# Optimization experiments

Hardware: AMD Instinct MI355X
Metric: run time of the kernel (lower is better)

## Reference

```python
import jax, jax.numpy as jnp
import numpy as np

V, E, H, L, B, T = 20000, 128, 192, 3, 256, 512


def _lstm_dir(x, W_ih, W_hh, b, reverse):
    """One direction of one LSTM layer. x: [B,T,I] -> (outputs [B,T,H], final h [B,H]).
    PyTorch gate order: i, f, g, o. b = b_ih + b_hh (summed, same math)."""
    gx = jnp.einsum('bti,gi->tbg', x, W_ih) + b  # [T,B,4H] input contributions, precomputed
    Wh = W_hh.T                                   # [H,4H]

    def step(carry, g):
        h, c = carry
        z = g + h @ Wh                            # [B,4H]
        i, f, gg, o = jnp.split(z, 4, axis=-1)
        c = jax.nn.sigmoid(f) * c + jax.nn.sigmoid(i) * jnp.tanh(gg)
        h = jax.nn.sigmoid(o) * jnp.tanh(c)
        return (h, c), h

    h0 = jnp.zeros((x.shape[0], H), x.dtype)
    (hT, _), hs = jax.lax.scan(step, (h0, h0), gx, reverse=reverse)
    return hs.transpose(1, 0, 2), hT


def setup_inputs() -> dict:
    key = jax.random.key(0)
    ks = jax.random.split(key, 12)
    k = 1.0 / np.sqrt(H)
    u = lambda kk, shape: jax.random.uniform(kk, shape, jnp.float32, -k, k)
    emb = jax.random.normal(ks[0], (V, E), jnp.float32)
    emb = emb.at[0].set(0.0)  # padding_idx=0
    return {
        'x': jax.random.randint(ks[1], (B, T), 0, V),
        'emb': emb,
        'W_ih0': u(ks[2], (2, 4 * H, E)),        # layer 0, [dir, 4H, E]
        'W_hh0': u(ks[3], (2, 4 * H, H)),
        'b0': u(ks[4], (2, 4 * H)) + u(ks[5], (2, 4 * H)),  # b_ih + b_hh
        'W_ih_r': u(ks[6], (L - 1, 2, 4 * H, 2 * H)),       # layers 1..2 take concat(fwd,bwd)
        'W_hh_r': u(ks[7], (L - 1, 2, 4 * H, H)),
        'b_r': u(ks[8], (L - 1, 2, 4 * H)) + u(ks[9], (L - 1, 2, 4 * H)),
        'fc_w': u(ks[10], (1, 2 * H)),
        'fc_b': u(ks[11], (1,)),
    }


def reference(x, emb, W_ih0, W_hh0, b0, W_ih_r, W_hh_r, b_r, fc_w, fc_b):
    h = emb[x]  # [B,T,E]
    hT_f = hT_b = None
    for l in range(L):
        if l == 0:
            Wi, Wh, bb = W_ih0, W_hh0, b0
        else:
            Wi, Wh, bb = W_ih_r[l - 1], W_hh_r[l - 1], b_r[l - 1]
        out_f, hT_f = _lstm_dir(h, Wi[0], Wh[0], bb[0], reverse=False)
        out_b, hT_b = _lstm_dir(h, Wi[1], Wh[1], bb[1], reverse=True)
        h = jnp.concatenate([out_f, out_b], axis=-1)  # [B,T,2H]
        # inter-layer dropout is inactive at inference
    last = jnp.concatenate([hT_f, hT_b], axis=-1)     # [B,2H]  (hidden[-2], hidden[-1])
    return last @ fc_w.T + fc_b                        # [B,1]
```

## Files before the change

### kernel.cpp

```cpp
#include <hip/hip_runtime.h>
#include <hip/hip_bf16.h>


typedef _Float16 f16;
typedef unsigned int u32;
typedef _Float16 f16x8 __attribute__((ext_vector_type(8)));
typedef float f32x4 __attribute__((ext_vector_type(4)));

__device__ __forceinline__ float sigm(float x) {
  float e = __builtin_amdgcn_exp2f(x * -1.44269504088896f);
  return __builtin_amdgcn_rcpf(1.0f + e);
}
__device__ __forceinline__ float tanh_(float x) {
  float e = __builtin_amdgcn_exp2f(x * -2.88539008177793f);
  return __builtin_fmaf(2.0f, __builtin_amdgcn_rcpf(1.0f + e), -1.0f);
}


__global__ void castk(const float* __restrict__ s, f16* __restrict__ d, int n) {
  int i = blockIdx.x * 256 + threadIdx.x;
  int st = gridDim.x * 256;
  for (; i < n; i += st) d[i] = (f16)s[i];
}

__global__ void castwhh(const float* __restrict__ src, f16* __restrict__ dst) {
  int o = blockIdx.x * 256 + threadIdx.x;
  int e = o & 7, rest = o >> 3;
  int l = rest & 63; rest >>= 6;
  int kk = rest % 6; rest /= 6;
  int g = rest & 3; rest >>= 2;
  int w = rest % 12; int dir = rest / 12;
  int lo16 = l & 15, lhi = l >> 4;
  dst[o] = (f16)src[(size_t)(dir * 768 + g * 192 + w * 16 + lo16) * 192 + kk * 32 + lhi * 8 + e];
}

__global__ void embedk(const int* __restrict__ x, const float* __restrict__ emb,
                       f16* __restrict__ A0) {
  int row = blockIdx.x * 8 + (threadIdx.x >> 5);
  int t = row >> 8, b = row & 255;
  int xi = x[b * 512 + t];
  int c = (threadIdx.x & 31) * 4;
  float4 v = *(const float4*)(emb + (size_t)xi * 128 + c);
  union { f16 h[4]; uint2 u; } p;
  p.h[0] = (f16)v.x; p.h[1] = (f16)v.y; p.h[2] = (f16)v.z; p.h[3] = (f16)v.w;
  *(uint2*)(A0 + (size_t)row * 128 + c) = p.u;
}

template <int KD>
__global__ __launch_bounds__(768)
void fusedk(const f16* __restrict__ in, const f16* __restrict__ Bt,
            const float* __restrict__ bias,
            const u32* __restrict__ gxR, u32* __restrict__ gxW,
            const f16* __restrict__ whh16,
            f16* __restrict__ outh, float* __restrict__ hT,
            f16* __restrict__ carh, float* __restrict__ carc,
            int c, int cg, int NC, int TC, int doLstm, int wOut, int wHT) {
  union SMem {
    struct { uint4 A[1024]; uint4 B[1536]; } g;
    f16 hb[2][16 * 200];
  };
  __shared__ __align__(16) SMem sm;
  const int wg = blockIdx.x;
  const int tid = threadIdx.x;
  const int l = tid & 63, w = tid >> 6;
  const int lo16 = l & 15, lhi = l >> 4;

  if (doLstm && wg < 32) {
    const int dir = wg & 1, bblk = wg >> 1;
    const int u0 = w * 16;
    const int bb = bblk * 16 + lhi * 4;
    const int dc = dir * 192;

    f16x8 wf[4][6];
#pragma unroll
    for (int g = 0; g < 4; ++g)
#pragma unroll
      for (int kk = 0; kk < 6; ++kk)
        wf[g][kk] = *(const f16x8*)(whh16 + ((((size_t)dir * 12 + w) * 4 + g) * 6 + kk) * 512 + l * 8);

    float cq[4];
    if (c == 0) {
      f16* hz = (f16*)sm.hb;
      for (int i = tid; i < 2 * 16 * 200; i += 768) hz[i] = (f16)0.f;
#pragma unroll
      for (int q = 0; q < 4; ++q) cq[q] = 0.f;
    } else {
#pragma unroll
      for (int q = 0; q < 4; ++q) {
        size_t ci = ((size_t)dir * 256 + bb + q) * 192 + u0 + lo16;
        cq[q] = carc[ci];
        sm.hb[0][(lhi * 4 + q) * 200 + u0 + lo16] = carh[ci];
      }
    }
    __syncthreads();

    u32 ga[8], gb[8];
    {
      const int tl0 = dir ? (TC - 1) : 0;
      size_t wb = ((((size_t)dir * TC + tl0) * 16 + bblk) * 12 + w) * 512;
#pragma unroll
      for (int k = 0; k < 8; ++k) ga[k] = gxR[wb + k * 64 + l];
    }
    const int tb0 = dir ? (511 - c * TC) : (c * TC);

#define RSTEP(S, CUR, NXT)                                                         \
  do {                                                                             \
    const int t = dir ? (tb0 - (S)) : (tb0 + (S));                                 \
    {                                                                              \
      int snx = ((S) + 1 < TC) ? (S) + 1 : (S);                                    \
      int tln = dir ? (TC - 1 - snx) : snx;                                        \
      size_t wb = ((((size_t)dir * TC + tln) * 16 + bblk) * 12 + w) * 512;         \
      _Pragma("unroll") for (int k = 0; k < 8; ++k) NXT[k] = gxR[wb + k * 64 + l]; \
    }                                                                              \
    f32x4 ac[4] = {};                                                              \
    {                                                                              \
      const f16* hcur = sm.hb[(S) & 1];                                            \
      _Pragma("unroll") for (int kk = 0; kk < 6; ++kk) {                           \
        f16x8 av = *(const f16x8*)(hcur + lo16 * 200 + kk * 32 + lhi * 8);         \
        ac[0] = __builtin_amdgcn_mfma_f32_16x16x32_f16(av, wf[0][kk], ac[0], 0, 0, 0); \
        ac[1] = __builtin_amdgcn_mfma_f32_16x16x32_f16(av, wf[1][kk], ac[1], 0, 0, 0); \
        ac[2] = __builtin_amdgcn_mfma_f32_16x16x32_f16(av, wf[2][kk], ac[2], 0, 0, 0); \
        ac[3] = __builtin_amdgcn_mfma_f32_16x16x32_f16(av, wf[3][kk], ac[3], 0, 0, 0); \
      }                                                                            \
    }                                                                              \
    float z[4][4];                                                                 \
    _Pragma("unroll") for (int k = 0; k < 8; ++k) {                                \
      union { u32 u; f16 h[2]; } p;                                                \
      p.u = CUR[k];                                                                \
      const int g_ = k >> 1, qq_ = k & 1;                                          \
      z[g_][2 * qq_] = ac[g_][2 * qq_] + (float)p.h[0];                            \
      z[g_][2 * qq_ + 1] = ac[g_][2 * qq_ + 1] + (float)p.h[1];                    \
    }                                                                              \
    f16* hnew = sm.hb[((S) + 1) & 1];                                              \
    _Pragma("unroll") for (int q = 0; q < 4; ++q) {                                \
      float iv = sigm(z[0][q]), fv = sigm(z[1][q]);                                \
      float gv = tanh_(z[2][q]), ov = sigm(z[3][q]);                               \
      cq[q] = fv * cq[q] + iv * gv;                                                \
      float hv = ov * tanh_(cq[q]);                                                \
      f16 hh = (f16)hv;                                                            \
      hnew[(lhi * 4 + q) * 200 + u0 + lo16] = hh;                                  \
      if (wOut) outh[((size_t)t * 256 + bb + q) * 384 + dc + u0 + lo16] = hh;      \
      if ((S) == TC - 1) {                                                         \
        size_t ci = ((size_t)dir * 256 + bb + q) * 192 + u0 + lo16;                \
        carh[ci] = hh;                                                             \
        carc[ci] = cq[q];                                                          \
        if (wHT && c == NC - 1) hT[ci] = hv;                                       \
      }                                                                            \
    }                                                                              \
    asm volatile("s_waitcnt lgkmcnt(0)" ::: "memory");                             \
    __builtin_amdgcn_s_barrier();                                                  \
    asm volatile("" ::: "memory");                                                 \
  } while (0)

    for (int s = 0; s < TC; s += 2) {
      RSTEP(s, ga, gb);
      RSTEP(s + 1, gb, ga);
    }
#undef RSTEP
    return;
  }

  if (cg >= NC) return;
  const int pool = doLstm ? 224 : 256;
  const int gid = doLstm ? wg - 32 : wg;
  const int RT = TC * 2;
  const int ntiles = RT * 8;
  const int tbf = cg * TC, tbb = 512 - (cg + 1) * TC;
  const int wm = (w >> 1) & 1;
  const int wmm = w / 6, wn = w % 6;
  (void)wm;
  constexpr int NKc = KD / 64;

  for (int tt = gid; tt < ntiles; tt += pool) {
    const int g = tt & 3;
    const int r = (tt >> 2) % RT;
    const int dir = (tt >> 2) / RT;
    const size_t ar0 = (size_t)(dir ? tbb : tbf) * 256 + r * 128;
    const int btr0 = dir * 768 + g * 192;

    float bj[2];
#pragma unroll
    for (int j = 0; j < 2; ++j) bj[j] = bias[btr0 + wn * 32 + j * 16 + lo16];

    f32x4 acc[4][2] = {};
    uint4 a0, a1, b0, b1;

#define LDG(ko_)                                                                   \
  do {                                                                             \
    { int idx = tid; int row = idx >> 3, sl = idx & 7; int ch = sl ^ (row & 7);    \
      a0 = *(const uint4*)(in + (ar0 + row) * KD + (ko_)*64 + ch * 8); }           \
    if (tid < 256) { int idx = tid + 768; int row = idx >> 3, sl = idx & 7;        \
      int ch = sl ^ (row & 7);                                                     \
      a1 = *(const uint4*)(in + (ar0 + row) * KD + (ko_)*64 + ch * 8); }           \
    { int idx = tid; int row = idx >> 3, sl = idx & 7; int ch = sl ^ (row & 7);    \
      b0 = *(const uint4*)(Bt + (size_t)(btr0 + row) * KD + (ko_)*64 + ch * 8); }  \
    { int idx = tid + 768; int row = idx >> 3, sl = idx & 7; int ch = sl ^ (row & 7); \
      b1 = *(const uint4*)(Bt + (size_t)(btr0 + row) * KD + (ko_)*64 + ch * 8); }  \
  } while (0)

    LDG(0);
    for (int ko = 0; ko < NKc; ++ko) {
      __syncthreads();
      sm.g.A[tid] = a0;
      if (tid < 256) sm.g.A[tid + 768] = a1;
      sm.g.B[tid] = b0;
      sm.g.B[tid + 768] = b1;
      __syncthreads();
      if (ko + 1 < NKc) LDG(ko + 1);
#pragma unroll
      for (int kk = 0; kk < 2; ++kk) {
        f16x8 af[4], bf[2];
#pragma unroll
        for (int i = 0; i < 4; ++i) {
          int rowA = wmm * 64 + i * 16 + lo16;
          int slA = (kk * 4 + lhi) ^ (rowA & 7);
          af[i] = *(const f16x8*)((const char*)sm.g.A + rowA * 128 + slA * 16);
        }
#pragma unroll
        for (int j = 0; j < 2; ++j) {
          int colB = wn * 32 + j * 16 + lo16;
          int slB = (kk * 4 + lhi) ^ (colB & 7);
          bf[j] = *(const f16x8*)((const char*)sm.g.B + colB * 128 + slB * 16);
        }
#pragma unroll
        for (int i = 0; i < 4; ++i)
#pragma unroll
          for (int j = 0; j < 2; ++j)
            acc[i][j] = __builtin_amdgcn_mfma_f32_16x16x32_f16(af[i], bf[j], acc[i][j], 0, 0, 0);
      }
    }
#undef LDG

#pragma unroll
    for (int i = 0; i < 4; ++i) {
      int rl = r * 128 + wmm * 64 + i * 16 + lhi * 4;
      int tl = rl >> 8;
      int b16 = (rl & 255) >> 4;
#pragma unroll
      for (int j = 0; j < 2; ++j) {
        int w12 = wn * 2 + j;
        size_t base = ((((size_t)dir * TC + tl) * 16 + b16) * 12 + w12) * 512;
#pragma unroll
        for (int qq = 0; qq < 2; ++qq) {
          union { f16 h[2]; u32 u; } p;
          p.h[0] = (f16)(acc[i][j][2 * qq] + bj[j]);
          p.h[1] = (f16)(acc[i][j][2 * qq + 1] + bj[j]);
          gxW[base + (g * 2 + qq) * 64 + l] = p.u;
        }
      }
    }
    __syncthreads();
  }
}

__global__ void fck(const float* __restrict__ hT, const float* __restrict__ w,
                    const float* __restrict__ fb, float* __restrict__ out) {
  int b = blockIdx.x * 64 + threadIdx.x;
  float a = fb[0];
#pragma unroll 4
  for (int u = 0; u < 192; ++u)
    a += w[u] * hT[(size_t)b * 192 + u] + w[192 + u] * hT[49152 + (size_t)b * 192 + u];
  out[b] = a;
}

extern "C" void kernel_launch(void* const* d_in, const int* in_sizes, int n_in,
                              void* d_out, int out_size, void* d_ws, size_t ws_size,
                              hipStream_t stream) {
  (void)in_sizes; (void)n_in; (void)out_size;
  const int* x = (const int*)d_in[0];
  const float* emb = (const float*)d_in[1];
  const float* Wih0 = (const float*)d_in[2];
  const float* Whh0 = (const float*)d_in[3];
  const float* b0 = (const float*)d_in[4];
  const float* Wihr = (const float*)d_in[5];
  const float* Whhr = (const float*)d_in[6];
  const float* br = (const float*)d_in[7];
  const float* fcw = (const float*)d_in[8];
  const float* fcb = (const float*)d_in[9];
  float* out = (float*)d_out;

  const size_t gxFull = 402653184ull;
  const size_t hB = 100663296ull;
  const size_t fixed = 2 * hB + 1179648 + 589824 + 393216 + 196608 + 393216;

  int NC;
  if (fixed + 2 * (gxFull / 32) <= ws_size) NC = 32;
  else if (fixed + 2 * (gxFull / 64) <= ws_size) NC = 64;
  else NC = 128;
  const int TC = 512 / NC;
  const size_t chunkB = gxFull / NC;

  char* ws = (char*)d_ws;
  u32* gxb[2] = {(u32*)ws, (u32*)(ws + chunkB)};
  size_t off = 2 * chunkB;
  f16* h0 = (f16*)(ws + off); off += hB;
  f16* h1 = (f16*)(ws + off); off += hB;
  f16* A0 = h1;
  f16* Bt = (f16*)(ws + off); off += 1179648ull;
  f16* whh16 = (f16*)(ws + off); off += 589824ull;
  float* hT = (float*)(ws + off); off += 393216ull;
  f16* carh = (f16*)(ws + off); off += 196608ull;
  float* carc = (float*)(ws + off); off += 393216ull;

  embedk<<<16384, 256, 0, stream>>>(x, emb, A0);

  for (int layer = 0; layer < 3; ++layer) {
    const f16* in = (layer == 0) ? A0 : (layer == 1 ? h0 : h1);
    f16* outp = (layer == 1) ? h1 : h0;
    const int wOut = (layer < 2) ? 1 : 0;
    const int wHT = (layer == 2) ? 1 : 0;
    const float* bias = (layer == 0) ? b0 : (br + (layer - 1) * 1536);

    if (layer == 0) {
      castk<<<192, 256, 0, stream>>>(Wih0, Bt, 196608);
      castwhh<<<1152, 256, 0, stream>>>(Whh0, whh16);
    } else {
      castk<<<1152, 256, 0, stream>>>(Wihr + (size_t)(layer - 1) * 589824, Bt, 589824);
      castwhh<<<1152, 256, 0, stream>>>(Whhr + (size_t)(layer - 1) * 294912, whh16);
    }

    if (layer == 0)
      fusedk<128><<<256, 768, 0, stream>>>(in, Bt, bias, gxb[0], gxb[0], whh16,
                                           outp, hT, carh, carc, 0, 0, NC, TC, 0, wOut, wHT);
    else
      fusedk<384><<<256, 768, 0, stream>>>(in, Bt, bias, gxb[0], gxb[0], whh16,
                                           outp, hT, carh, carc, 0, 0, NC, TC, 0, wOut, wHT);

    for (int c = 0; c < NC; ++c) {
      const u32* gR = gxb[c & 1];
      u32* gW = gxb[(c + 1) & 1];
      if (layer == 0)
        fusedk<128><<<256, 768, 0, stream>>>(in, Bt, bias, gR, gW, whh16,
                                             outp, hT, carh, carc, c, c + 1, NC, TC, 1, wOut, wHT);
      else
        fusedk<384><<<256, 768, 0, stream>>>(in, Bt, bias, gR, gW, whh16,
                                             outp, hT, carh, carc, c, c + 1, NC, TC, 1, wOut, wHT);
    }
  }

  fck<<<4, 64, 0, stream>>>(hT, fcw, fcb, out);
}
```

Measured before the change: 3.093 ms.

## Replace per-chunk kernel launches with persistent producer-consumer kernel using flag sync

Replaces the per-chunk launch loop (NC launches per layer) with one persistent kernel per layer. 32 blocks run the recurrence across all chunks, and the remaining 224 blocks compute input-gate GEMM tiles into a ring buffer of R chunks. The two groups coordinate through done/freed atomic counters. This removes launch overhead and the per-chunk carry spill and reload of h/c, and lets the GEMM run ahead of the recurrence. The cost is spin-waiting, a dependence on all blocks being co-resident (deadlock risk otherwise), and atomic loads on the gx reads.

After: 3.892 ms. +25.8%, slower.

```diff
diff --git a/kernel.cpp b/kernel.cpp
--- a/kernel.cpp
+++ b/kernel.cpp
@@ -6,6 +6,9 @@
 typedef unsigned int u32;
 typedef _Float16 f16x8 __attribute__((ext_vector_type(8)));
 typedef float f32x4 __attribute__((ext_vector_type(4)));
+
+#define ATL(p) __hip_atomic_load((p), __ATOMIC_RELAXED, __HIP_MEMORY_SCOPE_AGENT)
+#define ATS(p, v) __hip_atomic_store((p), (v), __ATOMIC_RELAXED, __HIP_MEMORY_SCOPE_AGENT)
 
 __device__ __forceinline__ float sigm(float x) {
   float e = __builtin_amdgcn_exp2f(x * -1.44269504088896f);
@@ -46,15 +49,18 @@
   *(uint2*)(A0 + (size_t)row * 128 + c) = p.u;
 }
 
+__global__ void zerok(int* __restrict__ p) {
+  if (threadIdx.x < 128) p[threadIdx.x] = 0;
+}
+
 template <int KD>
 __global__ __launch_bounds__(768)
-void fusedk(const f16* __restrict__ in, const f16* __restrict__ Bt,
-            const float* __restrict__ bias,
-            const u32* __restrict__ gxR, u32* __restrict__ gxW,
-            const f16* __restrict__ whh16,
-            f16* __restrict__ outh, float* __restrict__ hT,
-            f16* __restrict__ carh, float* __restrict__ carc,
-            int c, int cg, int NC, int TC, int doLstm, int wOut, int wHT) {
+void persistk(const f16* __restrict__ in, const f16* __restrict__ Bt,
+              const float* __restrict__ bias, u32* gxring,
+              const f16* __restrict__ whh16,
+              f16* __restrict__ outh, float* __restrict__ hT,
+              int* done, int* freed,
+              int R, int NC, int TC, int wOut, int wHT) {
   union SMem {
     struct { uint4 A[1024]; uint4 B[1536]; } g;
     f16 hb[2][16 * 200];
@@ -64,8 +70,10 @@
   const int tid = threadIdx.x;
   const int l = tid & 63, w = tid >> 6;
   const int lo16 = l & 15, lhi = l >> 4;
-
-  if (doLstm && wg < 32) {
+  const size_t chunkDw = (size_t)TC * 196608;
+  const int ntiles = 16 * TC;
+
+  if (wg < 32) {
     const int dir = wg & 1, bblk = wg >> 1;
     const int u0 = w * 16;
     const int bb = bblk * 16 + lhi * 4;
@@ -78,30 +86,24 @@
       for (int kk = 0; kk < 6; ++kk)
         wf[g][kk] = *(const f16x8*)(whh16 + ((((size_t)dir * 12 + w) * 4 + g) * 6 + kk) * 512 + l * 8);
 
-    float cq[4];
-    if (c == 0) {
+    {
       f16* hz = (f16*)sm.hb;
       for (int i = tid; i < 2 * 16 * 200; i += 768) hz[i] = (f16)0.f;
-#pragma unroll
-      for (int q = 0; q < 4; ++q) cq[q] = 0.f;
-    } else {
-#pragma unroll
-      for (int q = 0; q < 4; ++q) {
-        size_t ci = ((size_t)dir * 256 + bb + q) * 192 + u0 + lo16;
-        cq[q] = carc[ci];
-        sm.hb[0][(lhi * 4 + q) * 200 + u0 + lo16] = carh[ci];
+    }
+    __syncthreads();
+    float cq[4] = {0.f, 0.f, 0.f, 0.f};
+
+    for (int c = 0; c < NC; ++c) {
+      while (ATL(done + c) < ntiles) __builtin_amdgcn_s_sleep(8);
+      u32* gxR = gxring + (size_t)(c % R) * chunkDw;
+      u32 ga[8], gb[8];
+      {
+        const int tl0 = dir ? (TC - 1) : 0;
+        size_t wb = ((((size_t)dir * TC + tl0) * 16 + bblk) * 12 + w) * 512;
+#pragma unroll
+        for (int k = 0; k < 8; ++k) ga[k] = ATL(gxR + wb + k * 64 + l);
       }
-    }
-    __syncthreads();
-
-    u32 ga[8], gb[8];
-    {
-      const int tl0 = dir ? (TC - 1) : 0;
-      size_t wb = ((((size_t)dir * TC + tl0) * 16 + bblk) * 12 + w) * 512;
-#pragma unroll
-      for (int k = 0; k < 8; ++k) ga[k] = gxR[wb + k * 64 + l];
-    }
-    const int tb0 = dir ? (511 - c * TC) : (c * TC);
+      const int tb0 = dir ? (511 - c * TC) : (c * TC);
 
 #define RSTEP(S, CUR, NXT)                                                         \
   do {                                                                             \
@@ -110,7 +112,7 @@
       int snx = ((S) + 1 < TC) ? (S) + 1 : (S);                                    \
       int tln = dir ? (TC - 1 - snx) : snx;                                        \
       size_t wb = ((((size_t)dir * TC + tln) * 16 + bblk) * 12 + w) * 512;         \
-      _Pragma("unroll") for (int k = 0; k < 8; ++k) NXT[k] = gxR[wb + k * 64 + l]; \
+      _Pragma("unroll") for (int k = 0; k < 8; ++k) NXT[k] = ATL(gxR + wb + k * 64 + l); \
     }                                                                              \
     f32x4 ac[4] = {};                                                              \
     {                                                                              \
@@ -140,50 +142,52 @@
       f16 hh = (f16)hv;                                                            \
       hnew[(lhi * 4 + q) * 200 + u0 + lo16] = hh;                                  \
       if (wOut) outh[((size_t)t * 256 + bb + q) * 384 + dc + u0 + lo16] = hh;      \
-      if ((S) == TC - 1) {                                                         \
-        size_t ci = ((size_t)dir * 256 + bb + q) * 192 + u0 + lo16;                \
-        carh[ci] = hh;                                                             \
-        carc[ci] = cq[q];                                                          \
-        if (wHT && c == NC - 1) hT[ci] = hv;                                       \
-      }                                                                            \
+      if (wHT && c == NC - 1 && (S) == TC - 1)                                     \
+        hT[((size_t)dir * 256 + bb + q) * 192 + u0 + lo16] = hv;                   \
     }                                                                              \
     asm volatile("s_waitcnt lgkmcnt(0)" ::: "memory");                             \
     __builtin_amdgcn_s_barrier();                                                  \
     asm volatile("" ::: "memory");                                                 \
   } while (0)
 
-    for (int s = 0; s < TC; s += 2) {
-      RSTEP(s, ga, gb);
-      RSTEP(s + 1, gb, ga);
-    }
+      for (int s = 0; s < TC; s += 2) {
+        RSTEP(s, ga, gb);
+        RSTEP(s + 1, gb, ga);
+      }
 #undef RSTEP
+      if (tid == 0)
+        __hip_atomic_fetch_add(freed + c, 1, __ATOMIC_RELEASE, __HIP_MEMORY_SCOPE_AGENT);
+    }
     return;
   }
 
-  if (cg >= NC) return;
-  const int pool = doLstm ? 224 : 256;
-  const int gid = doLstm ? wg - 32 : wg;
-  const int RT = TC * 2;
-  const int ntiles = RT * 8;
-  const int tbf = cg * TC, tbb = 512 - (cg + 1) * TC;
-  const int wm = (w >> 1) & 1;
+  const int gid = wg - 32;
+  const int nblk = 4 * TC;
   const int wmm = w / 6, wn = w % 6;
-  (void)wm;
   constexpr int NKc = KD / 64;
-
-  for (int tt = gid; tt < ntiles; tt += pool) {
-    const int g = tt & 3;
-    const int r = (tt >> 2) % RT;
-    const int dir = (tt >> 2) / RT;
+  int kprev = -1;
+
+  for (int gtb = gid; gtb < NC * nblk; gtb += 224) {
+    const int k = gtb / nblk, blk = gtb % nblk;
+    const int dir = blk / (2 * TC), r = blk % (2 * TC);
+    if (k != kprev) {
+      if (k >= R)
+        while (ATL(freed + (k - R)) < 32) __builtin_amdgcn_s_sleep(8);
+      kprev = k;
+    }
+    u32* gxW = gxring + (size_t)(k % R) * chunkDw;
+    const int tbf = k * TC, tbb = 512 - (k + 1) * TC;
     const size_t ar0 = (size_t)(dir ? tbb : tbf) * 256 + r * 128;
-    const int btr0 = dir * 768 + g * 192;
-
-    float bj[2];
-#pragma unroll
-    for (int j = 0; j < 2; ++j) bj[j] = bias[btr0 + wn * 32 + j * 16 + lo16];
-
-    f32x4 acc[4][2] = {};
-    uint4 a0, a1, b0, b1;
+
+    for (int g = 0; g < 4; ++g) {
+      const int btr0 = dir * 768 + g * 192;
+
+      float bj[2];
+#pragma unroll
+      for (int j = 0; j < 2; ++j) bj[j] = bias[btr0 + wn * 32 + j * 16 + lo16];
+
+      f32x4 acc[4][2] = {};
+      uint4 a0, a1, b0, b1;
 
 #define LDG(ko_)                                                                   \
   do {                                                                             \
@@ -198,58 +202,60 @@
       b1 = *(const uint4*)(Bt + (size_t)(btr0 + row) * KD + (ko_)*64 + ch * 8); }  \
   } while (0)
 
-    LDG(0);
-    for (int ko = 0; ko < NKc; ++ko) {
-      __syncthreads();
-      sm.g.A[tid] = a0;
-      if (tid < 256) sm.g.A[tid + 768] = a1;
-      sm.g.B[tid] = b0;
-      sm.g.B[tid + 768] = b1;
-      __syncthreads();
-      if (ko + 1 < NKc) LDG(ko + 1);
-#pragma unroll
-      for (int kk = 0; kk < 2; ++kk) {
-        f16x8 af[4], bf[2];
-#pragma unroll
-        for (int i = 0; i < 4; ++i) {
-          int rowA = wmm * 64 + i * 16 + lo16;
-          int slA = (kk * 4 + lhi) ^ (rowA & 7);
-          af[i] = *(const f16x8*)((const char*)sm.g.A + rowA * 128 + slA * 16);
-        }
-#pragma unroll
-        for (int j = 0; j < 2; ++j) {
-          int colB = wn * 32 + j * 16 + lo16;
-          int slB = (kk * 4 + lhi) ^ (colB & 7);
-          bf[j] = *(const f16x8*)((const char*)sm.g.B + colB * 128 + slB * 16);
-        }
-#pragma unroll
-        for (int i = 0; i < 4; ++i)
-#pragma unroll
-          for (int j = 0; j < 2; ++j)
-            acc[i][j] = __builtin_amdgcn_mfma_f32_16x16x32_f16(af[i], bf[j], acc[i][j], 0, 0, 0);
-      }
-    }
-#undef LDG
-
-#pragma unroll
-    for (int i = 0; i < 4; ++i) {
-      int rl = r * 128 + wmm * 64 + i * 16 + lhi * 4;
-      int tl = rl >> 8;
-      int b16 = (rl & 255) >> 4;
-#pragma unroll
-      for (int j = 0; j < 2; ++j) {
-        int w12 = wn * 2 + j;
-        size_t base = ((((size_t)dir * TC + tl) * 16 + b16) * 12 + w12) * 512;
-#pragma unroll
-        for (int qq = 0; qq < 2; ++qq) {
-          union { f16 h[2]; u32 u; } p;
-          p.h[0] = (f16)(acc[i][j][2 * qq] + bj[j]);
-          p.h[1] = (f16)(acc[i][j][2 * qq + 1] + bj[j]);
-          gxW[base + (g * 2 + qq) * 64 + l] = p.u;
+      LDG(0);
+      for (int ko = 0; ko < NKc; ++ko) {
+        __syncthreads();
+        sm.g.A[tid] = a0;
+        if (tid < 256) sm.g.A[tid + 768] = a1;
+        sm.g.B[tid] = b0;
+        sm.g.B[tid + 768] = b1;
+        __syncthreads();
+        if (ko + 1 < NKc) LDG(ko + 1);
+#pragma unroll
+        for (int kk = 0; kk < 2; ++kk) {
+          f16x8 af[4], bf[2];
+#pragma unroll
+          for (int i = 0; i < 4; ++i) {
+            int rowA = wmm * 64 + i * 16 + lo16;
+            int slA = (kk * 4 + lhi) ^ (rowA & 7);
+            af[i] = *(const f16x8*)((const char*)sm.g.A + rowA * 128 + slA * 16);
+          }
+#pragma unroll
+          for (int j = 0; j < 2; ++j) {
+            int colB = wn * 32 + j * 16 + lo16;
+            int slB = (kk * 4 + lhi) ^ (colB & 7);
+            bf[j] = *(const f16x8*)((const char*)sm.g.B + colB * 128 + slB * 16);
+          }
+#pragma unroll
+          for (int i = 0; i < 4; ++i)
+#pragma unroll
+            for (int j = 0; j < 2; ++j)
+              acc[i][j] = __builtin_amdgcn_mfma_f32_16x16x32_f16(af[i], bf[j], acc[i][j], 0, 0, 0);
         }
       }
-    }
-    __syncthreads();
+#undef LDG
+
+#pragma unroll
+      for (int i = 0; i < 4; ++i) {
+        int rl = r * 128 + wmm * 64 + i * 16 + lhi * 4;
+        int tl = rl >> 8;
+        int b16 = (rl & 255) >> 4;
+#pragma unroll
+        for (int j = 0; j < 2; ++j) {
+          int w12 = wn * 2 + j;
+          size_t base = ((((size_t)dir * TC + tl) * 16 + b16) * 12 + w12) * 512;
+#pragma unroll
+          for (int qq = 0; qq < 2; ++qq) {
+            union { f16 h[2]; u32 u; } p;
+            p.h[0] = (f16)(acc[i][j][2 * qq] + bj[j]);
+            p.h[1] = (f16)(acc[i][j][2 * qq + 1] + bj[j]);
+            ATS(gxW + base + (g * 2 + qq) * 64 + l, p.u);
+          }
+        }
+      }
+      __syncthreads();
+    }
+    __hip_atomic_fetch_add(done + k, 4, __ATOMIC_RELEASE, __HIP_MEMORY_SCOPE_AGENT);
   }
 }
 
@@ -279,34 +285,36 @@
   const float* fcb = (const float*)d_in[9];
   float* out = (float*)d_out;
 
-  const size_t gxFull = 402653184ull;
   const size_t hB = 100663296ull;
-  const size_t fixed = 2 * hB + 1179648 + 589824 + 393216 + 196608 + 393216;
-
-  int NC;
-  if (fixed + 2 * (gxFull / 32) <= ws_size) NC = 32;
-  else if (fixed + 2 * (gxFull / 64) <= ws_size) NC = 64;
-  else NC = 128;
-  const int TC = 512 / NC;
-  const size_t chunkB = gxFull / NC;
+  const size_t fixedB = 2 * hB + 1179648ull + 589824ull + 393216ull + 4096ull;
+
+  int TC = 8, R = 2;
+  {
+    const int cT[3] = {16, 8, 8};
+    const int cR[3] = {2, 3, 2};
+    for (int i = 0; i < 3; ++i) {
+      size_t need = (size_t)cR[i] * cT[i] * 786432ull + fixedB;
+      if (need <= ws_size) { TC = cT[i]; R = cR[i]; break; }
+    }
+  }
+  const int NC = 512 / TC;
 
   char* ws = (char*)d_ws;
-  u32* gxb[2] = {(u32*)ws, (u32*)(ws + chunkB)};
-  size_t off = 2 * chunkB;
+  u32* gx = (u32*)ws;
+  size_t off = (size_t)R * TC * 786432ull;
   f16* h0 = (f16*)(ws + off); off += hB;
   f16* h1 = (f16*)(ws + off); off += hB;
   f16* A0 = h1;
   f16* Bt = (f16*)(ws + off); off += 1179648ull;
   f16* whh16 = (f16*)(ws + off); off += 589824ull;
   float* hT = (float*)(ws + off); off += 393216ull;
-  f16* carh = (f16*)(ws + off); off += 196608ull;
-  float* carc = (float*)(ws + off); off += 393216ull;
+  int* flags = (int*)(ws + off);
+  int* done = flags;
+  int* freed = flags + 64;
 
   embedk<<<16384, 256, 0, stream>>>(x, emb, A0);
 
   for (int layer = 0; layer < 3; ++layer) {
-    const f16* in = (layer == 0) ? A0 : (layer == 1 ? h0 : h1);
-    f16* outp = (layer == 1) ? h1 : h0;
     const int wOut = (layer < 2) ? 1 : 0;
     const int wHT = (layer == 2) ? 1 : 0;
     const float* bias = (layer == 0) ? b0 : (br + (layer - 1) * 1536);
@@ -318,24 +326,17 @@
       castk<<<1152, 256, 0, stream>>>(Wihr + (size_t)(layer - 1) * 589824, Bt, 589824);
       castwhh<<<1152, 256, 0, stream>>>(Whhr + (size_t)(layer - 1) * 294912, whh16);
     }
+    zerok<<<1, 128, 0, stream>>>(flags);
 
     if (layer == 0)
-      fusedk<128><<<256, 768, 0, stream>>>(in, Bt, bias, gxb[0], gxb[0], whh16,
-                                           outp, hT, carh, carc, 0, 0, NC, TC, 0, wOut, wHT);
+      persistk<128><<<256, 768, 0, stream>>>(A0, Bt, b0, gx, whh16, h0, hT,
+                                             done, freed, R, NC, TC, wOut, wHT);
+    else if (layer == 1)
+      persistk<384><<<256, 768, 0, stream>>>(h0, Bt, bias, gx, whh16, h1, hT,
+                                             done, freed, R, NC, TC, wOut, wHT);
     else
-      fusedk<384><<<256, 768, 0, stream>>>(in, Bt, bias, gxb[0], gxb[0], whh16,
-                                           outp, hT, carh, carc, 0, 0, NC, TC, 0, wOut, wHT);
-
-    for (int c = 0; c < NC; ++c) {
-      const u32* gR = gxb[c & 1];
-      u32* gW = gxb[(c + 1) & 1];
-      if (layer == 0)
-        fusedk<128><<<256, 768, 0, stream>>>(in, Bt, bias, gR, gW, whh16,
-                                             outp, hT, carh, carc, c, c + 1, NC, TC, 1, wOut, wHT);
-      else
-        fusedk<384><<<256, 768, 0, stream>>>(in, Bt, bias, gR, gW, whh16,
-                                             outp, hT, carh, carc, c, c + 1, NC, TC, 1, wOut, wHT);
-    }
+      persistk<384><<<256, 768, 0, stream>>>(h1, Bt, bias, gx, whh16, h0, hT,
+                                             done, freed, R, NC, TC, wOut, wHT);
   }
 
   fck<<<4, 64, 0, stream>>>(hT, fcw, fcb, out);
```

## Deepen gx prefetch to three steps, fuse gate reciprocals, shrink time chunks

Applied to the files above, without the earlier changes.

The recurrent LSTM loop now prefetches the precomputed input-gate values three steps ahead through four rotating register buffers instead of one step ahead. This hides global-load latency on the serial critical path. The gate math is restructured to merge the sigmoid and tanh reciprocals, so the i*g and o*tanh(c) products each need one rcp, and exponents are clamped to avoid overflow. The chunk sizing also changes: time chunks are now 16 or 8 steps, which means more chunks and more launches but less workspace per chunk, at the cost of extra registers.

New measurement: 3.737 ms. +20.8%, slower.

```diff
diff --git a/kernel.cpp b/kernel.cpp
--- a/kernel.cpp
+++ b/kernel.cpp
@@ -6,15 +6,6 @@
 typedef unsigned int u32;
 typedef _Float16 f16x8 __attribute__((ext_vector_type(8)));
 typedef float f32x4 __attribute__((ext_vector_type(4)));
-
-__device__ __forceinline__ float sigm(float x) {
-  float e = __builtin_amdgcn_exp2f(x * -1.44269504088896f);
-  return __builtin_amdgcn_rcpf(1.0f + e);
-}
-__device__ __forceinline__ float tanh_(float x) {
-  float e = __builtin_amdgcn_exp2f(x * -2.88539008177793f);
-  return __builtin_fmaf(2.0f, __builtin_amdgcn_rcpf(1.0f + e), -1.0f);
-}
 
 
 __global__ void castk(const float* __restrict__ s, f16* __restrict__ d, int n) {
@@ -64,6 +55,7 @@
   const int tid = threadIdx.x;
   const int l = tid & 63, w = tid >> 6;
   const int lo16 = l & 15, lhi = l >> 4;
+  const int TCm1 = TC - 1;
 
   if (doLstm && wg < 32) {
     const int dir = wg & 1, bblk = wg >> 1;
@@ -94,24 +86,27 @@
     }
     __syncthreads();
 
-    u32 ga[8], gb[8];
-    {
-      const int tl0 = dir ? (TC - 1) : 0;
-      size_t wb = ((((size_t)dir * TC + tl0) * 16 + bblk) * 12 + w) * 512;
-#pragma unroll
-      for (int k = 0; k < 8; ++k) ga[k] = gxR[wb + k * 64 + l];
-    }
+    u32 bA[8], bB[8], bC[8], bD[8];
+
+#define LOADSTEP(SL, BUF)                                                          \
+    do {                                                                           \
+      int sl_ = (SL) < TCm1 ? (SL) : TCm1;                                         \
+      int tl_ = dir ? (TCm1 - sl_) : sl_;                                          \
+      size_t wb_ = ((((size_t)dir * TC + tl_) * 16 + bblk) * 12 + w) * 512;        \
+      _Pragma("unroll") for (int k2 = 0; k2 < 8; ++k2)                             \
+        BUF[k2] = gxR[wb_ + k2 * 64 + l];                                          \
+    } while (0)
+
+    LOADSTEP(0, bA);
+    LOADSTEP(1, bB);
+    LOADSTEP(2, bC);
+
     const int tb0 = dir ? (511 - c * TC) : (c * TC);
 
 #define RSTEP(S, CUR, NXT)                                                         \
   do {                                                                             \
     const int t = dir ? (tb0 - (S)) : (tb0 + (S));                                 \
-    {                                                                              \
-      int snx = ((S) + 1 < TC) ? (S) + 1 : (S);                                    \
-      int tln = dir ? (TC - 1 - snx) : snx;                                        \
-      size_t wb = ((((size_t)dir * TC + tln) * 16 + bblk) * 12 + w) * 512;         \
-      _Pragma("unroll") for (int k = 0; k < 8; ++k) NXT[k] = gxR[wb + k * 64 + l]; \
-    }                                                                              \
+    LOADSTEP((S) + 3, NXT);                                                        \
     f32x4 ac[4] = {};                                                              \
     {                                                                              \
       const f16* hcur = sm.hb[(S) & 1];                                            \
@@ -124,23 +119,28 @@
       }                                                                            \
     }                                                                              \
     float z[4][4];                                                                 \
-    _Pragma("unroll") for (int k = 0; k < 8; ++k) {                                \
+    _Pragma("unroll") for (int k2 = 0; k2 < 8; ++k2) {                             \
       union { u32 u; f16 h[2]; } p;                                                \
-      p.u = CUR[k];                                                                \
-      const int g_ = k >> 1, qq_ = k & 1;                                          \
+      p.u = CUR[k2];                                                               \
+      const int g_ = k2 >> 1, qq_ = k2 & 1;                                        \
       z[g_][2 * qq_] = ac[g_][2 * qq_] + (float)p.h[0];                            \
       z[g_][2 * qq_ + 1] = ac[g_][2 * qq_ + 1] + (float)p.h[1];                    \
     }                                                                              \
     f16* hnew = sm.hb[((S) + 1) & 1];                                              \
     _Pragma("unroll") for (int q = 0; q < 4; ++q) {                                \
-      float iv = sigm(z[0][q]), fv = sigm(z[1][q]);                                \
-      float gv = tanh_(z[2][q]), ov = sigm(z[3][q]);                               \
-      cq[q] = fv * cq[q] + iv * gv;                                                \
-      float hv = ov * tanh_(cq[q]);                                                \
+      float ei = __builtin_amdgcn_exp2f(fminf(z[0][q] * -1.44269504f, 80.f));      \
+      float ef = __builtin_amdgcn_exp2f(fminf(z[1][q] * -1.44269504f, 80.f));      \
+      float eg = __builtin_amdgcn_exp2f(fminf(z[2][q] * -2.88539008f, 80.f));      \
+      float eo = __builtin_amdgcn_exp2f(fminf(z[3][q] * -1.44269504f, 80.f));      \
+      float ig = (1.f - eg) * __builtin_amdgcn_rcpf((1.f + eg) * (1.f + ei));      \
+      float fv = __builtin_amdgcn_rcpf(1.f + ef);                                  \
+      cq[q] = fv * cq[q] + ig;                                                     \
+      float ec = __builtin_amdgcn_exp2f(fminf(cq[q] * -2.88539008f, 80.f));        \
+      float hv = (1.f - ec) * __builtin_amdgcn_rcpf((1.f + ec) * (1.f + eo));      \
       f16 hh = (f16)hv;                                                            \
       hnew[(lhi * 4 + q) * 200 + u0 + lo16] = hh;                                  \
       if (wOut) outh[((size_t)t * 256 + bb + q) * 384 + dc + u0 + lo16] = hh;      \
-      if ((S) == TC - 1) {                                                         \
+      if ((S) == TCm1) {                                                           \
         size_t ci = ((size_t)dir * 256 + bb + q) * 192 + u0 + lo16;                \
         carh[ci] = hh;                                                             \
         carc[ci] = cq[q];                                                          \
@@ -152,11 +152,14 @@
     asm volatile("" ::: "memory");                                                 \
   } while (0)
 
-    for (int s = 0; s < TC; s += 2) {
-      RSTEP(s, ga, gb);
-      RSTEP(s + 1, gb, ga);
+    for (int s = 0; s < TC; s += 4) {
+      RSTEP(s, bA, bD);
+      RSTEP(s + 1, bB, bA);
+      RSTEP(s + 2, bC, bB);
+      RSTEP(s + 3, bD, bC);
     }
 #undef RSTEP
+#undef LOADSTEP
     return;
   }
 
@@ -166,9 +169,7 @@
   const int RT = TC * 2;
   const int ntiles = RT * 8;
   const int tbf = cg * TC, tbb = 512 - (cg + 1) * TC;
-  const int wm = (w >> 1) & 1;
   const int wmm = w / 6, wn = w % 6;
-  (void)wm;
   constexpr int NKc = KD / 64;
 
   for (int tt = gid; tt < ntiles; tt += pool) {
@@ -279,16 +280,12 @@
   const float* fcb = (const float*)d_in[9];
   float* out = (float*)d_out;
 
-  const size_t gxFull = 402653184ull;
   const size_t hB = 100663296ull;
-  const size_t fixed = 2 * hB + 1179648 + 589824 + 393216 + 196608 + 393216;
-
-  int NC;
-  if (fixed + 2 * (gxFull / 32) <= ws_size) NC = 32;
-  else if (fixed + 2 * (gxFull / 64) <= ws_size) NC = 64;
-  else NC = 128;
-  const int TC = 512 / NC;
-  const size_t chunkB = gxFull / NC;
+  const size_t fixedB = 2 * hB + 1179648ull + 589824ull + 393216ull + 196608ull + 393216ull;
+
+  int TC = (ws_size >= fixedB + 2ull * 16 * 786432ull) ? 16 : 8;
+  const int NC = 512 / TC;
+  const size_t chunkB = (size_t)TC * 786432ull;
 
   char* ws = (char*)d_ws;
   u32* gxb[2] = {(u32*)ws, (u32*)(ws + chunkB)};
```

## Shrink GEMM row tile, fold gate preactivations into MFMA accumulators, cap chunk size

Applied to the files above, without the earlier changes.

The input-projection GEMM tile shrinks from 128 to 64 rows per workgroup, so there are more tiles for the helper workgroups to share. The recurrent step now seeds the MFMA accumulators with the precomputed gate inputs instead of adding them afterwards. It also uses a strided output pointer and precomputed shared-memory offsets. Time-chunk size is capped at 16 steps (or 8 if the workspace is small), which means more chunk launches and smaller gx buffers. This is meant to give better overlap and load balance with the sequential LSTM, at the cost of less A/B reuse per tile and more kernel launches.

After: 2.779 ms. -10.1%, faster.

```diff
diff --git a/kernel.cpp b/kernel.cpp
--- a/kernel.cpp
+++ b/kernel.cpp
@@ -56,7 +56,7 @@
             f16* __restrict__ carh, float* __restrict__ carc,
             int c, int cg, int NC, int TC, int doLstm, int wOut, int wHT) {
   union SMem {
-    struct { uint4 A[1024]; uint4 B[1536]; } g;
+    struct { uint4 A[512]; uint4 B[1536]; } g;
     f16 hb[2][16 * 200];
   };
   __shared__ __align__(16) SMem sm;
@@ -64,12 +64,14 @@
   const int tid = threadIdx.x;
   const int l = tid & 63, w = tid >> 6;
   const int lo16 = l & 15, lhi = l >> 4;
+  const int TCm1 = TC - 1;
 
   if (doLstm && wg < 32) {
     const int dir = wg & 1, bblk = wg >> 1;
     const int u0 = w * 16;
     const int bb = bblk * 16 + lhi * 4;
     const int dc = dir * 192;
+    const int hb0 = lhi * 800 + u0 + lo16;
 
     f16x8 wf[4][6];
 #pragma unroll
@@ -94,25 +96,33 @@
     }
     __syncthreads();
 
+    const int tb0 = dir ? (511 - c * TC) : (c * TC);
+    f16* outp = outh + ((size_t)tb0 * 256 + bb) * 384 + dc + u0 + lo16;
+    const ptrdiff_t ostep = dir ? -(ptrdiff_t)98304 : (ptrdiff_t)98304;
+
     u32 ga[8], gb[8];
     {
-      const int tl0 = dir ? (TC - 1) : 0;
+      const int tl0 = dir ? TCm1 : 0;
       size_t wb = ((((size_t)dir * TC + tl0) * 16 + bblk) * 12 + w) * 512;
 #pragma unroll
-      for (int k = 0; k < 8; ++k) ga[k] = gxR[wb + k * 64 + l];
-    }
-    const int tb0 = dir ? (511 - c * TC) : (c * TC);
+      for (int k2 = 0; k2 < 8; ++k2) ga[k2] = gxR[wb + k2 * 64 + l];
+    }
 
 #define RSTEP(S, CUR, NXT)                                                         \
   do {                                                                             \
-    const int t = dir ? (tb0 - (S)) : (tb0 + (S));                                 \
     {                                                                              \
       int snx = ((S) + 1 < TC) ? (S) + 1 : (S);                                    \
-      int tln = dir ? (TC - 1 - snx) : snx;                                        \
+      int tln = dir ? (TCm1 - snx) : snx;                                          \
       size_t wb = ((((size_t)dir * TC + tln) * 16 + bblk) * 12 + w) * 512;         \
-      _Pragma("unroll") for (int k = 0; k < 8; ++k) NXT[k] = gxR[wb + k * 64 + l]; \
-    }                                                                              \
-    f32x4 ac[4] = {};                                                              \
+      _Pragma("unroll") for (int k2 = 0; k2 < 8; ++k2) NXT[k2] = gxR[wb + k2 * 64 + l]; \
+    }                                                                              \
+    f32x4 ac[4];                                                                   \
+    _Pragma("unroll") for (int g_ = 0; g_ < 4; ++g_) {                             \
+      union { u32 u; f16 h[2]; } p0, p1;                                           \
+      p0.u = CUR[2 * g_]; p1.u = CUR[2 * g_ + 1];                                  \
+      ac[g_][0] = (float)p0.h[0]; ac[g_][1] = (float)p0.h[1];                      \
+      ac[g_][2] = (float)p1.h[0]; ac[g_][3] = (float)p1.h[1];                      \
+    }                                                                              \
     {                                                                              \
       const f16* hcur = sm.hb[(S) & 1];                                            \
       _Pragma("unroll") for (int kk = 0; kk < 6; ++kk) {                           \
@@ -123,30 +133,23 @@
         ac[3] = __builtin_amdgcn_mfma_f32_16x16x32_f16(av, wf[3][kk], ac[3], 0, 0, 0); \
       }                                                                            \
     }                                                                              \
-    float z[4][4];                                                                 \
-    _Pragma("unroll") for (int k = 0; k < 8; ++k) {                                \
-      union { u32 u; f16 h[2]; } p;                                                \
-      p.u = CUR[k];                                                                \
-      const int g_ = k >> 1, qq_ = k & 1;                                          \
-      z[g_][2 * qq_] = ac[g_][2 * qq_] + (float)p.h[0];                            \
-      z[g_][2 * qq_ + 1] = ac[g_][2 * qq_ + 1] + (float)p.h[1];                    \
-    }                                                                              \
     f16* hnew = sm.hb[((S) + 1) & 1];                                              \
     _Pragma("unroll") for (int q = 0; q < 4; ++q) {                                \
-      float iv = sigm(z[0][q]), fv = sigm(z[1][q]);                                \
-      float gv = tanh_(z[2][q]), ov = sigm(z[3][q]);                               \
+      float iv = sigm(ac[0][q]), fv = sigm(ac[1][q]);                              \
+      float gv = tanh_(ac[2][q]), ov = sigm(ac[3][q]);                             \
       cq[q] = fv * cq[q] + iv * gv;                                                \
       float hv = ov * tanh_(cq[q]);                                                \
       f16 hh = (f16)hv;                                                            \
-      hnew[(lhi * 4 + q) * 200 + u0 + lo16] = hh;                                  \
-      if (wOut) outh[((size_t)t * 256 + bb + q) * 384 + dc + u0 + lo16] = hh;      \
-      if ((S) == TC - 1) {                                                         \
+      hnew[hb0 + q * 200] = hh;                                                    \
+      if (wOut) outp[q * 384] = hh;                                                \
+      if ((S) == TCm1) {                                                           \
         size_t ci = ((size_t)dir * 256 + bb + q) * 192 + u0 + lo16;                \
         carh[ci] = hh;                                                             \
         carc[ci] = cq[q];                                                          \
         if (wHT && c == NC - 1) hT[ci] = hv;                                       \
       }                                                                            \
     }                                                                              \
+    outp += ostep;                                                                 \
     asm volatile("s_waitcnt lgkmcnt(0)" ::: "memory");                             \
     __builtin_amdgcn_s_barrier();                                                  \
     asm volatile("" ::: "memory");                                                 \
@@ -163,56 +166,52 @@
   if (cg >= NC) return;
   const int pool = doLstm ? 224 : 256;
   const int gid = doLstm ? wg - 32 : wg;
-  const int RT = TC * 2;
+  const int RT = TC * 4;
   const int ntiles = RT * 8;
   const int tbf = cg * TC, tbb = 512 - (cg + 1) * TC;
-  const int wm = (w >> 1) & 1;
   const int wmm = w / 6, wn = w % 6;
-  (void)wm;
   constexpr int NKc = KD / 64;
 
   for (int tt = gid; tt < ntiles; tt += pool) {
     const int g = tt & 3;
     const int r = (tt >> 2) % RT;
     const int dir = (tt >> 2) / RT;
-    const size_t ar0 = (size_t)(dir ? tbb : tbf) * 256 + r * 128;
+    const size_t ar0 = (size_t)(dir ? tbb : tbf) * 256 + r * 64;
     const int btr0 = dir * 768 + g * 192;
 
     float bj[2];
 #pragma unroll
     for (int j = 0; j < 2; ++j) bj[j] = bias[btr0 + wn * 32 + j * 16 + lo16];
 
-    f32x4 acc[4][2] = {};
-    uint4 a0, a1, b0, b1;
+    f32x4 acc[2][2] = {};
+    uint4 a0v, b0v, b1v;
 
 #define LDG(ko_)                                                                   \
   do {                                                                             \
-    { int idx = tid; int row = idx >> 3, sl = idx & 7; int ch = sl ^ (row & 7);    \
-      a0 = *(const uint4*)(in + (ar0 + row) * KD + (ko_)*64 + ch * 8); }           \
-    if (tid < 256) { int idx = tid + 768; int row = idx >> 3, sl = idx & 7;        \
-      int ch = sl ^ (row & 7);                                                     \
-      a1 = *(const uint4*)(in + (ar0 + row) * KD + (ko_)*64 + ch * 8); }           \
-    { int idx = tid; int row = idx >> 3, sl = idx & 7; int ch = sl ^ (row & 7);    \
-      b0 = *(const uint4*)(Bt + (size_t)(btr0 + row) * KD + (ko_)*64 + ch * 8); }  \
-    { int idx = tid + 768; int row = idx >> 3, sl = idx & 7; int ch = sl ^ (row & 7); \
-      b1 = *(const uint4*)(Bt + (size_t)(btr0 + row) * KD + (ko_)*64 + ch * 8); }  \
+    if (tid < 512) {                                                               \
+      int row = tid >> 3, sl = tid & 7, ch = sl ^ (row & 7);                       \
+      a0v = *(const uint4*)(in + (ar0 + row) * KD + (ko_)*64 + ch * 8);            \
+    }                                                                              \
+    { int row = tid >> 3, sl = tid & 7, ch = sl ^ (row & 7);                       \
+      b0v = *(const uint4*)(Bt + (size_t)(btr0 + row) * KD + (ko_)*64 + ch * 8); } \
+    { int idx = tid + 768; int row = idx >> 3, sl = idx & 7, ch = sl ^ (row & 7);  \
+      b1v = *(const uint4*)(Bt + (size_t)(btr0 + row) * KD + (ko_)*64 + ch * 8); } \
   } while (0)
 
     LDG(0);
     for (int ko = 0; ko < NKc; ++ko) {
       __syncthreads();
-      sm.g.A[tid] = a0;
-      if (tid < 256) sm.g.A[tid + 768] = a1;
-      sm.g.B[tid] = b0;
-      sm.g.B[tid + 768] = b1;
+      if (tid < 512) sm.g.A[tid] = a0v;
+      sm.g.B[tid] = b0v;
+      sm.g.B[tid + 768] = b1v;
       __syncthreads();
       if (ko + 1 < NKc) LDG(ko + 1);
 #pragma unroll
       for (int kk = 0; kk < 2; ++kk) {
-        f16x8 af[4], bf[2];
-#pragma unroll
-        for (int i = 0; i < 4; ++i) {
-          int rowA = wmm * 64 + i * 16 + lo16;
+        f16x8 af[2], bf[2];
+#pragma unroll
+        for (int i = 0; i < 2; ++i) {
+          int rowA = wmm * 32 + i * 16 + lo16;
           int slA = (kk * 4 + lhi) ^ (rowA & 7);
           af[i] = *(const f16x8*)((const char*)sm.g.A + rowA * 128 + slA * 16);
         }
@@ -223,7 +222,7 @@
           bf[j] = *(const f16x8*)((const char*)sm.g.B + colB * 128 + slB * 16);
         }
 #pragma unroll
-        for (int i = 0; i < 4; ++i)
+        for (int i = 0; i < 2; ++i)
 #pragma unroll
           for (int j = 0; j < 2; ++j)
             acc[i][j] = __builtin_amdgcn_mfma_f32_16x16x32_f16(af[i], bf[j], acc[i][j], 0, 0, 0);
@@ -232,8 +231,8 @@
 #undef LDG
 
 #pragma unroll
-    for (int i = 0; i < 4; ++i) {
-      int rl = r * 128 + wmm * 64 + i * 16 + lhi * 4;
+    for (int i = 0; i < 2; ++i) {
+      int rl = r * 64 + wmm * 32 + i * 16 + lhi * 4;
       int tl = rl >> 8;
       int b16 = (rl & 255) >> 4;
 #pragma unroll
@@ -279,16 +278,12 @@
   const float* fcb = (const float*)d_in[9];
   float* out = (float*)d_out;
 
-  const size_t gxFull = 402653184ull;
   const size_t hB = 100663296ull;
-  const size_t fixed = 2 * hB + 1179648 + 589824 + 393216 + 196608 + 393216;
-
-  int NC;
-  if (fixed + 2 * (gxFull / 32) <= ws_size) NC = 32;
-  else if (fixed + 2 * (gxFull / 64) <= ws_size) NC = 64;
-  else NC = 128;
-  const int TC = 512 / NC;
-  const size_t chunkB = gxFull / NC;
+  const size_t fixedB = 2 * hB + 1179648ull + 589824ull + 393216ull + 196608ull + 393216ull;
+
+  int TC = (ws_size >= fixedB + 2ull * 16 * 786432ull) ? 16 : 8;
+  const int NC = 512 / TC;
+  const size_t chunkB = (size_t)TC * 786432ull;
 
   char* ws = (char*)d_ws;
   u32* gxb[2] = {(u32*)ws, (u32*)(ws + chunkB)};
```
